# Kernel tuning notes

Hardware: AMD Instinct MI355X
Metric: run time of the kernel (lower is better)

The kernel has to match this reference:

```python
import jax, jax.numpy as jnp
import numpy as np

B, S, DH, DF, DM = 32, 2048, 1024, 1024, 512


def setup_inputs() -> dict:
    key = jax.random.key(0)
    ks = jax.random.split(key, 7)
    s_h = 1.0 / np.sqrt(DH)
    s_f = 1.0 / np.sqrt(DF)
    s_m = 1.0 / np.sqrt(DM)
    return {
        "hidden_states": jax.random.normal(ks[0], (B, DH), jnp.float32),
        "feats": jax.random.normal(ks[1], (B, S, DF), jnp.float32),
        "W1h": jax.random.uniform(ks[2], (DM, DH), jnp.float32, -s_h, s_h),
        "b1h": jax.random.uniform(ks[3], (DM,), jnp.float32, -s_h, s_h),
        "W1f": jax.random.uniform(ks[4], (DM, DF), jnp.float32, -s_f, s_f),
        "b1f": jax.random.uniform(ks[5], (DM,), jnp.float32, -s_f, s_f),
        "w2": jax.random.uniform(ks[6], (DM,), jnp.float32, -s_m, s_m),
    }


def reference(hidden_states, feats, W1h, b1h, W1f, b1f, w2):
    # additive (Bahdanau) attention, single feature stream
    emb_h = hidden_states @ W1h.T + b1h                     # [B, DM]
    emb_f = jnp.einsum('bsd,md->bsm', feats, W1f) + b1f      # [B, S, DM]
    emb = jnp.tanh(emb_h[:, None, :] + emb_f)                # [B, S, DM]
    logits = jnp.einsum('bsm,m->bs', emb, w2)                # [B, S]
    probs = jax.nn.softmax(logits, axis=-1)                  # [B, S]
    context = jnp.einsum('bs,bsd->bd', probs, feats)         # [B, DF]
    # torch: cat(context, dim=1) -> [B, DF]; stack(probs, dim=1) -> [B, 1, S]
    return context, probs[:, None, :]
```

## Files before the change

### kernel.cpp

```cpp
#include <hip/hip_runtime.h>
#include <hip/hip_bf16.h>
#include <cstdint>
#include <cstddef>

#define B_   32
#define S_   2048
#define DH_  1024
#define DF_  1024
#define DM_  512
#define MTOT (B_ * S_)

typedef __attribute__((ext_vector_type(8))) short bf16x8;
typedef __attribute__((ext_vector_type(4))) float f32x4;

static __device__ __forceinline__ unsigned pack_bf16_2(float a, float b) {
    unsigned ua = __float_as_uint(a);
    unsigned ub = __float_as_uint(b);
    ua = (ua + 0x7FFFu + ((ua >> 16) & 1u)) >> 16;
    ub = (ub + 0x7FFFu + ((ub >> 16) & 1u)) >> 16;
    return ua | (ub << 16);
}

static __device__ __forceinline__ float tanh_fast(float x) {
    float e = __expf(2.0f * x);
    return 1.0f - 2.0f / (e + 1.0f);
}

__global__ __launch_bounds__(256) void k_embh(
    const float* __restrict__ hidden, const float* __restrict__ W1h,
    const float* __restrict__ b1h, const float* __restrict__ b1f,
    float* __restrict__ embh)
{
    int b = blockIdx.x;
    int t = threadIdx.x;
    const float4* h4 = (const float4*)(hidden + (size_t)b * DH_);
    for (int m = t; m < DM_; m += 256) {
        const float4* w4 = (const float4*)(W1h + (size_t)m * DH_);
        float s = 0.0f;
        #pragma unroll 4
        for (int i = 0; i < DH_ / 4; ++i) {
            float4 a = h4[i];
            float4 w = w4[i];
            s += a.x * w.x + a.y * w.y + a.z * w.z + a.w * w.w;
        }
        embh[b * DM_ + m] = s + b1h[m] + b1f[m];
    }
}

__global__ __launch_bounds__(256) void k_cvt_w1f(
    const float* __restrict__ w1f, unsigned short* __restrict__ out)
{
    int i = blockIdx.x * 256 + threadIdx.x;
    float4 v = ((const float4*)w1f)[i];
    uint2 o;
    o.x = pack_bf16_2(v.x, v.y);
    o.y = pack_bf16_2(v.z, v.w);
    ((uint2*)out)[i] = o;
}

__global__ __launch_bounds__(256) void k_gemm_logits(
    const float* __restrict__ feats, const unsigned short* __restrict__ w1fb,
    const float* __restrict__ embh, const float* __restrict__ w2,
    float* __restrict__ plog)
{
    __shared__ bf16x8 As[4 * 128];
    __shared__ bf16x8 Bs[4 * 128];

    const int t    = threadIdx.x;
    const int lane = t & 63;
    const int w    = t >> 6;
    const int wm   = w >> 1;
    const int wn   = w & 1;
    const int quad = lane >> 4;
    const int l16  = lane & 15;
    const int bx   = blockIdx.x;
    const int by   = blockIdx.y;

    const int sRow = t >> 1;
    const int sK   = (t & 1) * 16;
    const int c0   = sK >> 3;
    const float*          aG = feats + (size_t)(by * 128 + sRow) * DF_ + sK;
    const unsigned short* bG = w1fb  + (size_t)(bx * 128 + sRow) * DF_ + sK;

    f32x4 acc[4][4];
    const f32x4 zero = {0.0f, 0.0f, 0.0f, 0.0f};
    #pragma unroll
    for (int i = 0; i < 4; ++i)
        #pragma unroll
        for (int j = 0; j < 4; ++j) acc[i][j] = zero;

    for (int kt = 0; kt < DF_ / 32; ++kt) {
        float4 a0 = *(const float4*)(aG + kt * 32);
        float4 a1 = *(const float4*)(aG + kt * 32 + 4);
        float4 a2 = *(const float4*)(aG + kt * 32 + 8);
        float4 a3 = *(const float4*)(aG + kt * 32 + 12);
        uint4  b0 = *(const uint4*)(bG + kt * 32);
        uint4  b1 = *(const uint4*)(bG + kt * 32 + 8);

        __syncthreads();

        union { unsigned u[4]; bf16x8 v; } pa;
        pa.u[0] = pack_bf16_2(a0.x, a0.y);
        pa.u[1] = pack_bf16_2(a0.z, a0.w);
        pa.u[2] = pack_bf16_2(a1.x, a1.y);
        pa.u[3] = pack_bf16_2(a1.z, a1.w);
        As[c0 * 128 + sRow] = pa.v;
        pa.u[0] = pack_bf16_2(a2.x, a2.y);
        pa.u[1] = pack_bf16_2(a2.z, a2.w);
        pa.u[2] = pack_bf16_2(a3.x, a3.y);
        pa.u[3] = pack_bf16_2(a3.z, a3.w);
        As[(c0 + 1) * 128 + sRow] = pa.v;

        union { uint4 q; bf16x8 v; } pb;
        pb.q = b0;
        Bs[c0 * 128 + sRow] = pb.v;
        pb.q = b1;
        Bs[(c0 + 1) * 128 + sRow] = pb.v;

        __syncthreads();

        bf16x8 af[4], bfr[4];
        #pragma unroll
        for (int mi = 0; mi < 4; ++mi)
            af[mi] = As[quad * 128 + wm * 64 + mi * 16 + l16];
        #pragma unroll
        for (int nj = 0; nj < 4; ++nj)
            bfr[nj] = Bs[quad * 128 + wn * 64 + nj * 16 + l16];

        #pragma unroll
        for (int mi = 0; mi < 4; ++mi)
            #pragma unroll
            for (int nj = 0; nj < 4; ++nj)
                acc[mi][nj] = __builtin_amdgcn_mfma_f32_16x16x32_bf16(
                    af[mi], bfr[nj], acc[mi][nj], 0, 0, 0);
    }

    const int bIdx = by >> 4;
    float ew[4], wv[4];
    #pragma unroll
    for (int nj = 0; nj < 4; ++nj) {
        int c = bx * 128 + wn * 64 + nj * 16 + l16;
        ew[nj] = embh[bIdx * DM_ + c];
        wv[nj] = w2[c];
    }
    float* plw = plog + (size_t)(bx * 2 + wn) * MTOT + bIdx * S_;
    #pragma unroll
    for (int mi = 0; mi < 4; ++mi) {
        #pragma unroll
        for (int reg = 0; reg < 4; ++reg) {
            float p = 0.0f;
            #pragma unroll
            for (int nj = 0; nj < 4; ++nj) {
                float v = acc[mi][nj][reg] + ew[nj];
                p += tanh_fast(v) * wv[nj];
            }
            p += __shfl_xor(p, 1);
            p += __shfl_xor(p, 2);
            p += __shfl_xor(p, 4);
            p += __shfl_xor(p, 8);
            if (l16 == 0) {
                int rowl = wm * 64 + mi * 16 + quad * 4 + reg;
                int s = (by * 128 + rowl) & (S_ - 1);
                plw[s] = p;
            }
        }
    }
}

__global__ __launch_bounds__(256) void k_softmax(
    const float* __restrict__ plog, float* __restrict__ probs_out)
{
    int b = blockIdx.x;
    int t = threadIdx.x;
    float l[8];
    #pragma unroll
    for (int i = 0; i < 8; ++i) {
        int s = t + i * 256;
        float sum = 0.0f;
        #pragma unroll
        for (int p = 0; p < 8; ++p)
            sum += plog[(size_t)p * MTOT + b * S_ + s];
        l[i] = sum;
    }
    float mx = l[0];
    #pragma unroll
    for (int i = 1; i < 8; ++i) mx = fmaxf(mx, l[i]);
    #pragma unroll
    for (int off = 1; off < 64; off <<= 1) mx = fmaxf(mx, __shfl_xor(mx, off));
    __shared__ float redm[4];
    __shared__ float reds[4];
    int wid = t >> 6;
    if ((t & 63) == 0) redm[wid] = mx;
    __syncthreads();
    mx = fmaxf(fmaxf(redm[0], redm[1]), fmaxf(redm[2], redm[3]));

    float e[8];
    float es = 0.0f;
    #pragma unroll
    for (int i = 0; i < 8; ++i) {
        e[i] = __expf(l[i] - mx);
        es += e[i];
    }
    #pragma unroll
    for (int off = 1; off < 64; off <<= 1) es += __shfl_xor(es, off);
    if ((t & 63) == 0) reds[wid] = es;
    __syncthreads();
    es = reds[0] + reds[1] + reds[2] + reds[3];
    float inv = 1.0f / es;
    #pragma unroll
    for (int i = 0; i < 8; ++i)
        probs_out[b * S_ + t + i * 256] = e[i] * inv;
}

__global__ __launch_bounds__(256) void k_context(
    const float* __restrict__ feats, const float* __restrict__ probs,
    float* __restrict__ ctx)
{
    int d  = blockIdx.x * 256 + threadIdx.x;
    int b  = blockIdx.y;
    int s0 = blockIdx.z * 256;
    const float* f  = feats + ((size_t)b * S_ + s0) * DF_ + d;
    const float* pr = probs + b * S_ + s0;
    float acc = 0.0f;
    #pragma unroll 4
    for (int i = 0; i < 256; ++i)
        acc += pr[i] * f[(size_t)i * DF_];
    atomicAdd(&ctx[b * DF_ + d], acc);
}

extern "C" void kernel_launch(void* const* d_in, const int* in_sizes, int n_in,
                              void* d_out, int out_size, void* d_ws, size_t ws_size,
                              hipStream_t stream)
{
    const float* hidden = (const float*)d_in[0];
    const float* feats  = (const float*)d_in[1];
    const float* W1h    = (const float*)d_in[2];
    const float* b1h    = (const float*)d_in[3];
    const float* W1f    = (const float*)d_in[4];
    const float* b1f    = (const float*)d_in[5];
    const float* w2     = (const float*)d_in[6];

    float* out   = (float*)d_out;
    float* ctx   = out;
    float* probs = out + B_ * DF_;

    char* ws = (char*)d_ws;
    float*          embh = (float*)ws;
    unsigned short* w1fb = (unsigned short*)(ws + (64 << 10));
    float*          plog = (float*)(ws + (64 << 10) + (1 << 20));

    hipMemsetAsync(ctx, 0, B_ * DF_ * sizeof(float), stream);

    k_embh<<<dim3(B_), 256, 0, stream>>>(hidden, W1h, b1h, b1f, embh);
    k_cvt_w1f<<<dim3((DM_ * DF_ / 4) / 256), 256, 0, stream>>>(W1f, w1fb);
    k_gemm_logits<<<dim3(DM_ / 128, MTOT / 128), 256, 0, stream>>>(
        feats, w1fb, embh, w2, plog);
    k_softmax<<<dim3(B_), 256, 0, stream>>>(plog, probs);
    k_context<<<dim3(DF_ / 256, B_, 8), 256, 0, stream>>>(feats, probs, ctx);
}
```

Before: 599.7 us.

## Restructure logits GEMM with 256x128 tiles, 32x32 MFMA, double buffering, grouped raster

The logits GEMM now uses 256-row tiles with 32x32x16 bf16 MFMAs, double-buffered LDS, register prefetch of the next A tile and direct global-to-LDS loads for W1f. Blocks are rasterized in panels so feats rows are reused across column tiles. Separately, the embh kernel is split across more blocks with a shuffle reduction, bf16 rounding is simplified to round-half-up, and context atomics are replaced by partial buffers plus a reduction kernel. This aims to cut LDS/global traffic and sync stalls, at the cost of higher register pressure and an extra launch.

```diff
diff --git a/kernel.cpp b/kernel.cpp
--- a/kernel.cpp
+++ b/kernel.cpp
@@ -10,15 +10,21 @@
 #define DM_  512
 #define MTOT (B_ * S_)
 
-typedef __attribute__((ext_vector_type(8))) short bf16x8;
-typedef __attribute__((ext_vector_type(4))) float f32x4;
-
-static __device__ __forceinline__ unsigned pack_bf16_2(float a, float b) {
-    unsigned ua = __float_as_uint(a);
-    unsigned ub = __float_as_uint(b);
-    ua = (ua + 0x7FFFu + ((ua >> 16) & 1u)) >> 16;
-    ub = (ub + 0x7FFFu + ((ub >> 16) & 1u)) >> 16;
-    return ua | (ub << 16);
+typedef __attribute__((ext_vector_type(8)))  short bf16x8;
+typedef __attribute__((ext_vector_type(16))) float f32x16;
+
+#define AS1 __attribute__((address_space(1)))
+#define AS3 __attribute__((address_space(3)))
+
+static __device__ __forceinline__ void load_lds16(const void* g, void* l) {
+    __builtin_amdgcn_global_load_lds((const AS1 unsigned*)g, (AS3 unsigned*)l,
+                                     16, 0, 0);
+}
+
+static __device__ __forceinline__ unsigned pack_rhu(float a, float b) {
+    unsigned ua = (__float_as_uint(a) + 0x8000u) >> 16;
+    unsigned ub = (__float_as_uint(b) + 0x8000u) & 0xFFFF0000u;
+    return ua | ub;
 }
 
 static __device__ __forceinline__ float tanh_fast(float x) {
@@ -31,20 +37,24 @@
     const float* __restrict__ b1h, const float* __restrict__ b1f,
     float* __restrict__ embh)
 {
-    int b = blockIdx.x;
-    int t = threadIdx.x;
-    const float4* h4 = (const float4*)(hidden + (size_t)b * DH_);
-    for (int m = t; m < DM_; m += 256) {
-        const float4* w4 = (const float4*)(W1h + (size_t)m * DH_);
-        float s = 0.0f;
-        #pragma unroll 4
-        for (int i = 0; i < DH_ / 4; ++i) {
-            float4 a = h4[i];
-            float4 w = w4[i];
-            s += a.x * w.x + a.y * w.y + a.z * w.z + a.w * w.w;
-        }
+    int b  = blockIdx.x;
+    int mg = blockIdx.y;
+    int t  = threadIdx.x;
+    int m  = mg * 64 + (t >> 2);
+    int kp = (t & 3) * 256;
+    const float4* h4 = (const float4*)(hidden + (size_t)b * DH_ + kp);
+    const float4* w4 = (const float4*)(W1h + (size_t)m * DH_ + kp);
+    float s = 0.0f;
+    #pragma unroll 8
+    for (int i = 0; i < 64; ++i) {
+        float4 a = h4[i];
+        float4 w = w4[i];
+        s += a.x * w.x + a.y * w.y + a.z * w.z + a.w * w.w;
+    }
+    s += __shfl_xor(s, 1);
+    s += __shfl_xor(s, 2);
+    if ((t & 3) == 0)
         embh[b * DM_ + m] = s + b1h[m] + b1f[m];
-    }
 }
 
 __global__ __launch_bounds__(256) void k_cvt_w1f(
@@ -53,115 +63,128 @@
     int i = blockIdx.x * 256 + threadIdx.x;
     float4 v = ((const float4*)w1f)[i];
     uint2 o;
-    o.x = pack_bf16_2(v.x, v.y);
-    o.y = pack_bf16_2(v.z, v.w);
+    o.x = pack_rhu(v.x, v.y);
+    o.y = pack_rhu(v.z, v.w);
     ((uint2*)out)[i] = o;
 }
 
-__global__ __launch_bounds__(256) void k_gemm_logits(
+__global__ __launch_bounds__(256, 2) void k_gemm_logits(
     const float* __restrict__ feats, const unsigned short* __restrict__ w1fb,
     const float* __restrict__ embh, const float* __restrict__ w2,
     float* __restrict__ plog)
 {
-    __shared__ bf16x8 As[4 * 128];
-    __shared__ bf16x8 Bs[4 * 128];
+    __shared__ bf16x8 As[2][4 * 256];
+    __shared__ bf16x8 Bs[2][4 * 128];
 
     const int t    = threadIdx.x;
     const int lane = t & 63;
     const int w    = t >> 6;
     const int wm   = w >> 1;
     const int wn   = w & 1;
-    const int quad = lane >> 4;
-    const int l16  = lane & 15;
-    const int bx   = blockIdx.x;
-    const int by   = blockIdx.y;
-
-    const int sRow = t >> 1;
-    const int sK   = (t & 1) * 16;
-    const int c0   = sK >> 3;
-    const float*          aG = feats + (size_t)(by * 128 + sRow) * DF_ + sK;
-    const unsigned short* bG = w1fb  + (size_t)(bx * 128 + sRow) * DF_ + sK;
-
-    f32x4 acc[4][4];
-    const f32x4 zero = {0.0f, 0.0f, 0.0f, 0.0f};
-    #pragma unroll
-    for (int i = 0; i < 4; ++i)
-        #pragma unroll
-        for (int j = 0; j < 4; ++j) acc[i][j] = zero;
+    const int l32  = lane & 31;
+    const int half = lane >> 5;
+
+    const int blk   = blockIdx.x;
+    const int panel = blk >> 5;
+    const int sub   = blk & 31;
+    const int bx    = sub >> 3;
+    const int by    = panel * 8 + (sub & 7);
+
+    const float* aG = feats + (size_t)(by * 256 + t) * DF_;
+
+    const int s0 = (w * 2 + 0) * 64 + lane;
+    const int s1 = s0 + 64;
+    const unsigned short* bG0 =
+        w1fb + (size_t)(bx * 128 + (s0 & 127)) * DF_ + (s0 >> 7) * 8;
+    const unsigned short* bG1 =
+        w1fb + (size_t)(bx * 128 + (s1 & 127)) * DF_ + (s1 >> 7) * 8;
+    const int ldsSlot0 = (w * 2 + 0) * 64;
+    const int ldsSlot1 = (w * 2 + 1) * 64;
+
+    f32x16 acc[4][2];
+    #pragma unroll
+    for (int mi = 0; mi < 4; ++mi)
+        #pragma unroll
+        for (int nj = 0; nj < 2; ++nj)
+            #pragma unroll
+            for (int r = 0; r < 16; ++r) acc[mi][nj][r] = 0.0f;
+
+    float4 ar[8];
+    #pragma unroll
+    for (int j = 0; j < 8; ++j) ar[j] = ((const float4*)aG)[j];
+    load_lds16(bG0, &Bs[0][ldsSlot0]);
+    load_lds16(bG1, &Bs[0][ldsSlot1]);
 
     for (int kt = 0; kt < DF_ / 32; ++kt) {
-        float4 a0 = *(const float4*)(aG + kt * 32);
-        float4 a1 = *(const float4*)(aG + kt * 32 + 4);
-        float4 a2 = *(const float4*)(aG + kt * 32 + 8);
-        float4 a3 = *(const float4*)(aG + kt * 32 + 12);
-        uint4  b0 = *(const uint4*)(bG + kt * 32);
-        uint4  b1 = *(const uint4*)(bG + kt * 32 + 8);
+        const int cur = kt & 1;
+        const int nxt = cur ^ 1;
+
+        #pragma unroll
+        for (int c = 0; c < 4; ++c) {
+            union { unsigned u[4]; bf16x8 v; } pa;
+            pa.u[0] = pack_rhu(ar[2 * c].x,     ar[2 * c].y);
+            pa.u[1] = pack_rhu(ar[2 * c].z,     ar[2 * c].w);
+            pa.u[2] = pack_rhu(ar[2 * c + 1].x, ar[2 * c + 1].y);
+            pa.u[3] = pack_rhu(ar[2 * c + 1].z, ar[2 * c + 1].w);
+            As[cur][c * 256 + t] = pa.v;
+        }
+
+        if (kt + 1 < DF_ / 32) {
+            const float4* an = (const float4*)(aG + (kt + 1) * 32);
+            #pragma unroll
+            for (int j = 0; j < 8; ++j) ar[j] = an[j];
+        }
 
         __syncthreads();
 
-        union { unsigned u[4]; bf16x8 v; } pa;
-        pa.u[0] = pack_bf16_2(a0.x, a0.y);
-        pa.u[1] = pack_bf16_2(a0.z, a0.w);
-        pa.u[2] = pack_bf16_2(a1.x, a1.y);
-        pa.u[3] = pack_bf16_2(a1.z, a1.w);
-        As[c0 * 128 + sRow] = pa.v;
-        pa.u[0] = pack_bf16_2(a2.x, a2.y);
-        pa.u[1] = pack_bf16_2(a2.z, a2.w);
-        pa.u[2] = pack_bf16_2(a3.x, a3.y);
-        pa.u[3] = pack_bf16_2(a3.z, a3.w);
-        As[(c0 + 1) * 128 + sRow] = pa.v;
-
-        union { uint4 q; bf16x8 v; } pb;
-        pb.q = b0;
-        Bs[c0 * 128 + sRow] = pb.v;
-        pb.q = b1;
-        Bs[(c0 + 1) * 128 + sRow] = pb.v;
-
-        __syncthreads();
-
-        bf16x8 af[4], bfr[4];
-        #pragma unroll
-        for (int mi = 0; mi < 4; ++mi)
-            af[mi] = As[quad * 128 + wm * 64 + mi * 16 + l16];
-        #pragma unroll
-        for (int nj = 0; nj < 4; ++nj)
-            bfr[nj] = Bs[quad * 128 + wn * 64 + nj * 16 + l16];
-
-        #pragma unroll
-        for (int mi = 0; mi < 4; ++mi)
-            #pragma unroll
-            for (int nj = 0; nj < 4; ++nj)
-                acc[mi][nj] = __builtin_amdgcn_mfma_f32_16x16x32_bf16(
-                    af[mi], bfr[nj], acc[mi][nj], 0, 0, 0);
-    }
-
-    const int bIdx = by >> 4;
-    float ew[4], wv[4];
-    #pragma unroll
-    for (int nj = 0; nj < 4; ++nj) {
-        int c = bx * 128 + wn * 64 + nj * 16 + l16;
-        ew[nj] = embh[bIdx * DM_ + c];
+        if (kt + 1 < DF_ / 32) {
+            load_lds16(bG0 + (kt + 1) * 32, &Bs[nxt][ldsSlot0]);
+            load_lds16(bG1 + (kt + 1) * 32, &Bs[nxt][ldsSlot1]);
+        }
+
+        #pragma unroll
+        for (int h = 0; h < 2; ++h) {
+            const int c = h * 2 + half;
+            bf16x8 af[4], bfr[2];
+            #pragma unroll
+            for (int mi = 0; mi < 4; ++mi)
+                af[mi] = As[cur][c * 256 + wm * 128 + mi * 32 + l32];
+            #pragma unroll
+            for (int nj = 0; nj < 2; ++nj)
+                bfr[nj] = Bs[cur][c * 128 + wn * 64 + nj * 32 + l32];
+            #pragma unroll
+            for (int mi = 0; mi < 4; ++mi)
+                #pragma unroll
+                for (int nj = 0; nj < 2; ++nj)
+                    acc[mi][nj] = __builtin_amdgcn_mfma_f32_32x32x16_bf16(
+                        af[mi], bfr[nj], acc[mi][nj], 0, 0, 0);
+        }
+    }
+
+    const int b     = by >> 3;
+    const int sbase = (by & 7) * 256 + wm * 128;
+    float ew[2], wv[2];
+    #pragma unroll
+    for (int nj = 0; nj < 2; ++nj) {
+        int c = bx * 128 + wn * 64 + nj * 32 + l32;
+        ew[nj] = embh[b * DM_ + c];
         wv[nj] = w2[c];
     }
-    float* plw = plog + (size_t)(bx * 2 + wn) * MTOT + bIdx * S_;
+    float* plw = plog + (size_t)(bx * 2 + wn) * MTOT + b * S_;
     #pragma unroll
     for (int mi = 0; mi < 4; ++mi) {
         #pragma unroll
-        for (int reg = 0; reg < 4; ++reg) {
-            float p = 0.0f;
-            #pragma unroll
-            for (int nj = 0; nj < 4; ++nj) {
-                float v = acc[mi][nj][reg] + ew[nj];
-                p += tanh_fast(v) * wv[nj];
-            }
+        for (int reg = 0; reg < 16; ++reg) {
+            float p = tanh_fast(acc[mi][0][reg] + ew[0]) * wv[0]
+                    + tanh_fast(acc[mi][1][reg] + ew[1]) * wv[1];
             p += __shfl_xor(p, 1);
             p += __shfl_xor(p, 2);
             p += __shfl_xor(p, 4);
             p += __shfl_xor(p, 8);
-            if (l16 == 0) {
-                int rowl = wm * 64 + mi * 16 + quad * 4 + reg;
-                int s = (by * 128 + rowl) & (S_ - 1);
-                plw[s] = p;
+            p += __shfl_xor(p, 16);
+            if (l32 == 0) {
+                int row = mi * 32 + (reg & 3) + 8 * (reg >> 2) + 4 * half;
+                plw[sbase + row] = p;
             }
         }
     }
@@ -214,18 +237,30 @@
 
 __global__ __launch_bounds__(256) void k_context(
     const float* __restrict__ feats, const float* __restrict__ probs,
-    float* __restrict__ ctx)
+    float* __restrict__ ctxp)
 {
     int d  = blockIdx.x * 256 + threadIdx.x;
     int b  = blockIdx.y;
-    int s0 = blockIdx.z * 256;
+    int z  = blockIdx.z;
+    int s0 = z * 256;
     const float* f  = feats + ((size_t)b * S_ + s0) * DF_ + d;
     const float* pr = probs + b * S_ + s0;
     float acc = 0.0f;
     #pragma unroll 4
     for (int i = 0; i < 256; ++i)
         acc += pr[i] * f[(size_t)i * DF_];
-    atomicAdd(&ctx[b * DF_ + d], acc);
+    ctxp[((size_t)z * B_ + b) * DF_ + d] = acc;
+}
+
+__global__ __launch_bounds__(256) void k_ctx_red(
+    const float* __restrict__ ctxp, float* __restrict__ ctx)
+{
+    int i = blockIdx.x * 256 + threadIdx.x;
+    float s = 0.0f;
+    #pragma unroll
+    for (int z = 0; z < 8; ++z)
+        s += ctxp[(size_t)z * B_ * DF_ + i];
+    ctx[i] = s;
 }
 
 extern "C" void kernel_launch(void* const* d_in, const int* in_sizes, int n_in,
@@ -248,13 +283,13 @@
     float*          embh = (float*)ws;
     unsigned short* w1fb = (unsigned short*)(ws + (64 << 10));
     float*          plog = (float*)(ws + (64 << 10) + (1 << 20));
-
-    hipMemsetAsync(ctx, 0, B_ * DF_ * sizeof(float), stream);
-
-    k_embh<<<dim3(B_), 256, 0, stream>>>(hidden, W1h, b1h, b1f, embh);
+    float*          ctxp = (float*)(ws + (64 << 10) + (3 << 20));
+
+    k_embh<<<dim3(B_, DM_ / 64), 256, 0, stream>>>(hidden, W1h, b1h, b1f, embh);
     k_cvt_w1f<<<dim3((DM_ * DF_ / 4) / 256), 256, 0, stream>>>(W1f, w1fb);
-    k_gemm_logits<<<dim3(DM_ / 128, MTOT / 128), 256, 0, stream>>>(
+    k_gemm_logits<<<dim3((MTOT / 256) * (DM_ / 128)), 256, 0, stream>>>(
         feats, w1fb, embh, w2, plog);
     k_softmax<<<dim3(B_), 256, 0, stream>>>(plog, probs);
-    k_context<<<dim3(DF_ / 256, B_, 8), 256, 0, stream>>>(feats, probs, ctx);
-}
+    k_context<<<dim3(DF_ / 256, B_, 8), 256, 0, stream>>>(feats, probs, ctxp);
+    k_ctx_red<<<dim3(B_ * DF_ / 256), 256, 0, stream>>>(ctxp, ctx);
+}
```

Result: faster. 587.9 us (-2.0%).

## Pre-convert feats to bf16, use direct-to-LDS loads, swizzle GEMM grid

Applied to the files above, without the earlier changes.

When the workspace is large enough, feats is converted to bf16 once. The GEMM then streams bf16 tiles straight into LDS with global_load_lds, and the context pass reads the bf16 copy instead of fp32. This cuts the GEMM's in-loop conversion work and the context pass's read traffic, at the cost of an extra conversion pass over the whole tensor and bf16 rounding in the context output. Other changes: GEMM blocks are remapped into panels for better L2 reuse, the embh kernel gets a split-K layout, and the context atomics are replaced by partial sums plus a separate reduction kernel.

```diff
diff --git a/kernel.cpp b/kernel.cpp
--- a/kernel.cpp
+++ b/kernel.cpp
@@ -13,12 +13,18 @@
 typedef __attribute__((ext_vector_type(8))) short bf16x8;
 typedef __attribute__((ext_vector_type(4))) float f32x4;
 
-static __device__ __forceinline__ unsigned pack_bf16_2(float a, float b) {
-    unsigned ua = __float_as_uint(a);
-    unsigned ub = __float_as_uint(b);
-    ua = (ua + 0x7FFFu + ((ua >> 16) & 1u)) >> 16;
-    ub = (ub + 0x7FFFu + ((ub >> 16) & 1u)) >> 16;
-    return ua | (ub << 16);
+#define AS1 __attribute__((address_space(1)))
+#define AS3 __attribute__((address_space(3)))
+
+static __device__ __forceinline__ void load_lds16(const void* g, void* l) {
+    __builtin_amdgcn_global_load_lds((const AS1 unsigned*)g, (AS3 unsigned*)l,
+                                     16, 0, 0);
+}
+
+static __device__ __forceinline__ unsigned pack_rhu(float a, float b) {
+    unsigned ua = (__float_as_uint(a) + 0x8000u) >> 16;
+    unsigned ub = (__float_as_uint(b) + 0x8000u) & 0xFFFF0000u;
+    return ua | ub;
 }
 
 static __device__ __forceinline__ float tanh_fast(float x) {
@@ -31,35 +37,42 @@
     const float* __restrict__ b1h, const float* __restrict__ b1f,
     float* __restrict__ embh)
 {
-    int b = blockIdx.x;
-    int t = threadIdx.x;
-    const float4* h4 = (const float4*)(hidden + (size_t)b * DH_);
-    for (int m = t; m < DM_; m += 256) {
-        const float4* w4 = (const float4*)(W1h + (size_t)m * DH_);
-        float s = 0.0f;
-        #pragma unroll 4
-        for (int i = 0; i < DH_ / 4; ++i) {
-            float4 a = h4[i];
-            float4 w = w4[i];
-            s += a.x * w.x + a.y * w.y + a.z * w.z + a.w * w.w;
-        }
+    int b  = blockIdx.x;
+    int mg = blockIdx.y;
+    int t  = threadIdx.x;
+    int m  = mg * 64 + (t >> 2);
+    int kp = (t & 3) * 256;
+    const float4* h4 = (const float4*)(hidden + (size_t)b * DH_ + kp);
+    const float4* w4 = (const float4*)(W1h + (size_t)m * DH_ + kp);
+    float s = 0.0f;
+    #pragma unroll 8
+    for (int i = 0; i < 64; ++i) {
+        float4 a = h4[i];
+        float4 w = w4[i];
+        s += a.x * w.x + a.y * w.y + a.z * w.z + a.w * w.w;
+    }
+    s += __shfl_xor(s, 1);
+    s += __shfl_xor(s, 2);
+    if ((t & 3) == 0)
         embh[b * DM_ + m] = s + b1h[m] + b1f[m];
-    }
-}
-
-__global__ __launch_bounds__(256) void k_cvt_w1f(
-    const float* __restrict__ w1f, unsigned short* __restrict__ out)
-{
-    int i = blockIdx.x * 256 + threadIdx.x;
-    float4 v = ((const float4*)w1f)[i];
-    uint2 o;
-    o.x = pack_bf16_2(v.x, v.y);
-    o.y = pack_bf16_2(v.z, v.w);
-    ((uint2*)out)[i] = o;
-}
-
-__global__ __launch_bounds__(256) void k_gemm_logits(
-    const float* __restrict__ feats, const unsigned short* __restrict__ w1fb,
+}
+
+__global__ __launch_bounds__(256) void k_cvt(
+    const float* __restrict__ src, unsigned short* __restrict__ dst)
+{
+    size_t i = (size_t)blockIdx.x * 256 + threadIdx.x;
+    float4 a = ((const float4*)src)[2 * i];
+    float4 b = ((const float4*)src)[2 * i + 1];
+    uint4 r;
+    r.x = pack_rhu(a.x, a.y);
+    r.y = pack_rhu(a.z, a.w);
+    r.z = pack_rhu(b.x, b.y);
+    r.w = pack_rhu(b.z, b.w);
+    ((uint4*)dst)[i] = r;
+}
+
+__global__ __launch_bounds__(256) void k_gemm_bf(
+    const unsigned short* __restrict__ fb, const unsigned short* __restrict__ wb,
     const float* __restrict__ embh, const float* __restrict__ w2,
     float* __restrict__ plog)
 {
@@ -73,14 +86,21 @@
     const int wn   = w & 1;
     const int quad = lane >> 4;
     const int l16  = lane & 15;
-    const int bx   = blockIdx.x;
-    const int by   = blockIdx.y;
-
-    const int sRow = t >> 1;
-    const int sK   = (t & 1) * 16;
-    const int c0   = sK >> 3;
-    const float*          aG = feats + (size_t)(by * 128 + sRow) * DF_ + sK;
-    const unsigned short* bG = w1fb  + (size_t)(bx * 128 + sRow) * DF_ + sK;
+
+    const int blk   = blockIdx.x;
+    const int panel = blk >> 5;
+    const int sub   = blk & 31;
+    const int bx    = sub >> 3;
+    const int by    = panel * 8 + (sub & 7);
+
+    const unsigned short* aG0 = fb + ((size_t)(by * 128) + lane) * DF_ + w * 8;
+    const unsigned short* aG1 = aG0 + (size_t)64 * DF_;
+    const unsigned short* bG0 = wb + ((size_t)(bx * 128) + lane) * DF_ + w * 8;
+    const unsigned short* bG1 = bG0 + (size_t)64 * DF_;
+    bf16x8* ldsA0 = &As[w * 128];
+    bf16x8* ldsA1 = &As[w * 128 + 64];
+    bf16x8* ldsB0 = &Bs[w * 128];
+    bf16x8* ldsB1 = &Bs[w * 128 + 64];
 
     f32x4 acc[4][4];
     const f32x4 zero = {0.0f, 0.0f, 0.0f, 0.0f};
@@ -90,33 +110,11 @@
         for (int j = 0; j < 4; ++j) acc[i][j] = zero;
 
     for (int kt = 0; kt < DF_ / 32; ++kt) {
-        float4 a0 = *(const float4*)(aG + kt * 32);
-        float4 a1 = *(const float4*)(aG + kt * 32 + 4);
-        float4 a2 = *(const float4*)(aG + kt * 32 + 8);
-        float4 a3 = *(const float4*)(aG + kt * 32 + 12);
-        uint4  b0 = *(const uint4*)(bG + kt * 32);
-        uint4  b1 = *(const uint4*)(bG + kt * 32 + 8);
-
         __syncthreads();
-
-        union { unsigned u[4]; bf16x8 v; } pa;
-        pa.u[0] = pack_bf16_2(a0.x, a0.y);
-        pa.u[1] = pack_bf16_2(a0.z, a0.w);
-        pa.u[2] = pack_bf16_2(a1.x, a1.y);
-        pa.u[3] = pack_bf16_2(a1.z, a1.w);
-        As[c0 * 128 + sRow] = pa.v;
-        pa.u[0] = pack_bf16_2(a2.x, a2.y);
-        pa.u[1] = pack_bf16_2(a2.z, a2.w);
-        pa.u[2] = pack_bf16_2(a3.x, a3.y);
-        pa.u[3] = pack_bf16_2(a3.z, a3.w);
-        As[(c0 + 1) * 128 + sRow] = pa.v;
-
-        union { uint4 q; bf16x8 v; } pb;
-        pb.q = b0;
-        Bs[c0 * 128 + sRow] = pb.v;
-        pb.q = b1;
-        Bs[(c0 + 1) * 128 + sRow] = pb.v;
-
+        load_lds16(aG0 + kt * 32, ldsA0);
+        load_lds16(aG1 + kt * 32, ldsA1);
+        load_lds16(bG0 + kt * 32, ldsB0);
+        load_lds16(bG1 + kt * 32, ldsB1);
         __syncthreads();
 
         bf16x8 af[4], bfr[4];
@@ -150,10 +148,8 @@
         for (int reg = 0; reg < 4; ++reg) {
             float p = 0.0f;
             #pragma unroll
-            for (int nj = 0; nj < 4; ++nj) {
-                float v = acc[mi][nj][reg] + ew[nj];
-                p += tanh_fast(v) * wv[nj];
-            }
+            for (int nj = 0; nj < 4; ++nj)
+                p += tanh_fast(acc[mi][nj][reg] + ew[nj]) * wv[nj];
             p += __shfl_xor(p, 1);
             p += __shfl_xor(p, 2);
             p += __shfl_xor(p, 4);
@@ -167,6 +163,116 @@
     }
 }
 
+__global__ __launch_bounds__(256) void k_gemm_f32(
+    const float* __restrict__ feats, const unsigned short* __restrict__ w1fb,
+    const float* __restrict__ embh, const float* __restrict__ w2,
+    float* __restrict__ plog)
+{
+    __shared__ bf16x8 As[4 * 128];
+    __shared__ bf16x8 Bs[4 * 128];
+
+    const int t    = threadIdx.x;
+    const int lane = t & 63;
+    const int w    = t >> 6;
+    const int wm   = w >> 1;
+    const int wn   = w & 1;
+    const int quad = lane >> 4;
+    const int l16  = lane & 15;
+    const int blk   = blockIdx.x;
+    const int panel = blk >> 5;
+    const int sub   = blk & 31;
+    const int bx    = sub >> 3;
+    const int by    = panel * 8 + (sub & 7);
+
+    const int sRow = t >> 1;
+    const int sK   = (t & 1) * 16;
+    const int c0   = sK >> 3;
+    const float*          aG = feats + (size_t)(by * 128 + sRow) * DF_ + sK;
+    const unsigned short* bG = w1fb  + (size_t)(bx * 128 + sRow) * DF_ + sK;
+
+    f32x4 acc[4][4];
+    const f32x4 zero = {0.0f, 0.0f, 0.0f, 0.0f};
+    #pragma unroll
+    for (int i = 0; i < 4; ++i)
+        #pragma unroll
+        for (int j = 0; j < 4; ++j) acc[i][j] = zero;
+
+    for (int kt = 0; kt < DF_ / 32; ++kt) {
+        float4 a0 = *(const float4*)(aG + kt * 32);
+        float4 a1 = *(const float4*)(aG + kt * 32 + 4);
+        float4 a2 = *(const float4*)(aG + kt * 32 + 8);
+        float4 a3 = *(const float4*)(aG + kt * 32 + 12);
+        uint4  b0 = *(const uint4*)(bG + kt * 32);
+        uint4  b1 = *(const uint4*)(bG + kt * 32 + 8);
+
+        __syncthreads();
+
+        union { unsigned u[4]; bf16x8 v; } pa;
+        pa.u[0] = pack_rhu(a0.x, a0.y);
+        pa.u[1] = pack_rhu(a0.z, a0.w);
+        pa.u[2] = pack_rhu(a1.x, a1.y);
+        pa.u[3] = pack_rhu(a1.z, a1.w);
+        As[c0 * 128 + sRow] = pa.v;
+        pa.u[0] = pack_rhu(a2.x, a2.y);
+        pa.u[1] = pack_rhu(a2.z, a2.w);
+        pa.u[2] = pack_rhu(a3.x, a3.y);
+        pa.u[3] = pack_rhu(a3.z, a3.w);
+        As[(c0 + 1) * 128 + sRow] = pa.v;
+
+        union { uint4 q; bf16x8 v; } pb;
+        pb.q = b0;
+        Bs[c0 * 128 + sRow] = pb.v;
+        pb.q = b1;
+        Bs[(c0 + 1) * 128 + sRow] = pb.v;
+
+        __syncthreads();
+
+        bf16x8 af[4], bfr[4];
+        #pragma unroll
+        for (int mi = 0; mi < 4; ++mi)
+            af[mi] = As[quad * 128 + wm * 64 + mi * 16 + l16];
+        #pragma unroll
+        for (int nj = 0; nj < 4; ++nj)
+            bfr[nj] = Bs[quad * 128 + wn * 64 + nj * 16 + l16];
+
+        #pragma unroll
+        for (int mi = 0; mi < 4; ++mi)
+            #pragma unroll
+            for (int nj = 0; nj < 4; ++nj)
+                acc[mi][nj] = __builtin_amdgcn_mfma_f32_16x16x32_bf16(
+                    af[mi], bfr[nj], acc[mi][nj], 0, 0, 0);
+    }
+
+    const int bIdx = by >> 4;
+    float ew[4], wv[4];
+    #pragma unroll
+    for (int nj = 0; nj < 4; ++nj) {
+        int c = bx * 128 + wn * 64 + nj * 16 + l16;
+        ew[nj] = embh[bIdx * DM_ + c];
+        wv[nj] = w2[c];
+    }
+    float* plw = plog + (size_t)(bx * 2 + wn) * MTOT + bIdx * S_;
+    #pragma unroll
+    for (int mi = 0; mi < 4; ++mi) {
+        #pragma unroll
+        for (int reg = 0; reg < 4; ++reg) {
+            float p = 0.0f;
+            #pragma unroll
+            for (int nj = 0; nj < 4; ++nj)
+                p += tanh_fast(acc[mi][nj][reg] + ew[nj]) * wv[nj];
+            p += __shfl_xor(p, 1);
+            p += __shfl_xor(p, 2);
+            p += __shfl_xor(p, 4);
+            p += __shfl_xor(p, 8);
+            if (l16 == 0) {
+                int rowl = wm * 64 + mi * 16 + quad * 4 + reg;
+                int s = (by * 128 + rowl) & (S_ - 1);
+                plw[s] = p;
+            }
+        }
+    }
+}
+
 __global__ __launch_bounds__(256) void k_softmax(
     const float* __restrict__ plog, float* __restrict__ probs_out)
 {
@@ -212,20 +318,54 @@
         probs_out[b * S_ + t + i * 256] = e[i] * inv;
 }
 
-__global__ __launch_bounds__(256) void k_context(
+__global__ __launch_bounds__(256) void k_context_bf(
+    const unsigned short* __restrict__ fb, const float* __restrict__ probs,
+    float* __restrict__ ctxp)
+{
+    int dp = blockIdx.x * 256 + threadIdx.x;
+    int b  = blockIdx.y;
+    int z  = blockIdx.z;
+    const unsigned* f  = (const unsigned*)(fb + ((size_t)b * S_ + z * 256) * DF_) + dp;
+    const float*    pr = probs + b * S_ + z * 256;
+    float a0 = 0.0f, a1 = 0.0f;
+    #pragma unroll 4
+    for (int i = 0; i < 256; ++i) {
+        unsigned v = f[(size_t)i * (DF_ / 2)];
+        float lo = __uint_as_float(v << 16);
+        float hi = __uint_as_float(v & 0xFFFF0000u);
+        float p = pr[i];
+        a0 += p * lo;
+        a1 += p * hi;
+    }
+    float2* o = (float2*)(ctxp + ((size_t)z * B_ + b) * DF_) + dp;
+    *o = make_float2(a0, a1);
+}
+
+__global__ __launch_bounds__(256) void k_context_f32(
     const float* __restrict__ feats, const float* __restrict__ probs,
-    float* __restrict__ ctx)
+    float* __restrict__ ctxp)
 {
     int d  = blockIdx.x * 256 + threadIdx.x;
     int b  = blockIdx.y;
-    int s0 = blockIdx.z * 256;
-    const float* f  = feats + ((size_t)b * S_ + s0) * DF_ + d;
-    const float* pr = probs + b * S_ + s0;
+    int z  = blockIdx.z;
+    const float* f  = feats + ((size_t)b * S_ + z * 256) * DF_ + d;
+    const float* pr = probs + b * S_ + z * 256;
     float acc = 0.0f;
     #pragma unroll 4
     for (int i = 0; i < 256; ++i)
         acc += pr[i] * f[(size_t)i * DF_];
-    atomicAdd(&ctx[b * DF_ + d], acc);
+    ctxp[((size_t)z * B_ + b) * DF_ + d] = acc;
+}
+
+__global__ __launch_bounds__(256) void k_ctx_red(
+    const float* __restrict__ ctxp, float* __restrict__ ctx)
+{
+    int i = blockIdx.x * 256 + threadIdx.x;
+    float s = 0.0f;
+    #pragma unroll
+    for (int z = 0; z < 8; ++z)
+        s += ctxp[(size_t)z * B_ * DF_ + i];
+    ctx[i] = s;
 }
 
 extern "C" void kernel_launch(void* const* d_in, const int* in_sizes, int n_in,
@@ -245,16 +385,28 @@
     float* probs = out + B_ * DF_;
 
     char* ws = (char*)d_ws;
-    float*          embh = (float*)ws;
-    unsigned short* w1fb = (unsigned short*)(ws + (64 << 10));
-    float*          plog = (float*)(ws + (64 << 10) + (1 << 20));
-
-    hipMemsetAsync(ctx, 0, B_ * DF_ * sizeof(float), stream);
-
-    k_embh<<<dim3(B_), 256, 0, stream>>>(hidden, W1h, b1h, b1f, embh);
-    k_cvt_w1f<<<dim3((DM_ * DF_ / 4) / 256), 256, 0, stream>>>(W1f, w1fb);
-    k_gemm_logits<<<dim3(DM_ / 128, MTOT / 128), 256, 0, stream>>>(
-        feats, w1fb, embh, w2, plog);
-    k_softmax<<<dim3(B_), 256, 0, stream>>>(plog, probs);
-    k_context<<<dim3(DF_ / 256, B_, 8), 256, 0, stream>>>(feats, probs, ctx);
-}
+    float*          embh  = (float*)ws;
+    unsigned short* w1fb  = (unsigned short*)(ws + (64 << 10));
+    float*          plog  = (float*)(ws + (64 << 10) + (1 << 20));
+    float*          ctxp  = (float*)(ws + (64 << 10) + (3 << 20));
+    unsigned short* featb = (unsigned short*)(ws + (8 << 20));
+
+    const bool big_ws = ws_size >= ((size_t)8 << 20) + ((size_t)B_ * S_ * DF_ * 2);
+
+    k_embh<<<dim3(B_, DM_ / 64), 256, 0, stream>>>(hidden, W1h, b1h, b1f, embh);
+    k_cvt<<<dim3((DM_ * DF_ / 8) / 256), 256, 0, stream>>>(W1f, w1fb);
+
+    if (big_ws) {
+        k_cvt<<<dim3(((size_t)MTOT * DF_ / 8) / 256), 256, 0, stream>>>(feats, featb);
+        k_gemm_bf<<<dim3((MTOT / 128) * (DM_ / 128)), 256, 0, stream>>>(
+            featb, w1fb, embh, w2, plog);
+        k_softmax<<<dim3(B_), 256, 0, stream>>>(plog, probs);
+        k_context_bf<<<dim3(DF_ / 512, B_, 8), 256, 0, stream>>>(featb, probs, ctxp);
+    } else {
+        k_gemm_f32<<<dim3((MTOT / 128) * (DM_ / 128)), 256, 0, stream>>>(
+            feats, w1fb, embh, w2, plog);
+        k_softmax<<<dim3(B_), 256, 0, stream>>>(plog, probs);
+        k_context_f32<<<dim3(DF_ / 256, B_, 8), 256, 0, stream>>>(feats, probs, ctxp);
+    }
+    k_ctx_red<<<dim3(B_ * DF_ / 256), 256, 0, stream>>>(ctxp, ctx);
+}
```

New measurement: 574.7 us. 4.2% less time.
